# Kernel optimization log

Hardware: AMD Instinct MI355X
Metric: run time of the kernel (lower is better)

## Reference

```python
import jax, jax.numpy as jnp
import numpy as np

B, V, D, K = 32, 4096, 64, 512


def setup_inputs() -> dict:
    key = jax.random.key(0)
    k1, k2 = jax.random.split(key)
    z_e = jax.random.normal(k1, (B, V, D), dtype=jnp.float32)
    # nn.Embedding weight initialized uniform(-1/K, 1/K)
    emb = jax.random.uniform(k2, (K, D), dtype=jnp.float32, minval=-1.0 / K, maxval=1.0 / K)
    return {"z_e": z_e, "emb": emb}


def reference(z_e, emb):
    b, v, d = z_e.shape
    flat = z_e.reshape(-1, d)  # [N, D], N = B*V
    # Squared Euclidean distances via dot-product expansion.
    # torch.cdist returns sqrt of this, but argmin is identical (monotone sqrt).
    d2 = (
        jnp.sum(flat * flat, axis=-1, keepdims=True)  # [N, 1]
        - 2.0 * flat @ emb.T                          # [N, K]
        + jnp.sum(emb * emb, axis=-1)                 # [K]
    )
    indices = jnp.argmin(d2, axis=1)                  # [N]
    z_q = emb[indices].reshape(z_e.shape)             # [B, V, D]
    z_q_st = z_e + jax.lax.stop_gradient(z_q - z_e)   # straight-through
    return z_q_st, z_q, indices.reshape(b, v)
```

## Files before the change

### kernel.cpp

```cpp
#include <hip/hip_runtime.h>


#define VQ_N (32 * 4096)
#define VQ_D 64
#define VQ_K 512

__device__ __forceinline__ float freeze(float x) {
  asm volatile("" : "+v"(x));
  return x;
}

__global__ __launch_bounds__(256) void vq_norms_kernel(
    const float* __restrict__ emb, float* __restrict__ nrm) {
  int k = blockIdx.x * blockDim.x + threadIdx.x;
  if (k < VQ_K) {
    const float* e = emb + k * VQ_D;
    float r0 = freeze(e[0] * e[0]), r1 = freeze(e[1] * e[1]);
    float r2 = freeze(e[2] * e[2]), r3 = freeze(e[3] * e[3]);
    float r4 = freeze(e[4] * e[4]), r5 = freeze(e[5] * e[5]);
    float r6 = freeze(e[6] * e[6]), r7 = freeze(e[7] * e[7]);
#pragma unroll
    for (int i = 8; i < VQ_D; i += 8) {
      r0 += freeze(e[i + 0] * e[i + 0]); r1 += freeze(e[i + 1] * e[i + 1]);
      r2 += freeze(e[i + 2] * e[i + 2]); r3 += freeze(e[i + 3] * e[i + 3]);
      r4 += freeze(e[i + 4] * e[i + 4]); r5 += freeze(e[i + 5] * e[i + 5]);
      r6 += freeze(e[i + 6] * e[i + 6]); r7 += freeze(e[i + 7] * e[i + 7]);
    }
    nrm[k] = ((r0 + r1) + (r2 + r3)) + ((r4 + r5) + (r6 + r7));
  }
}

__global__ __launch_bounds__(256) void vq_main_kernel(
    const float* __restrict__ z_e, const float* __restrict__ emb,
    const float* __restrict__ nrm, float* __restrict__ out_st,
    float* __restrict__ out_q, float* __restrict__ out_idx) {
  __shared__ float4 z_lds[16][64];
  __shared__ float s_val[256];
  __shared__ int s_idx[256];
  __shared__ int s_best[64];

  const int tid = threadIdx.x;
  const int lane = tid & 63;
  const int chunk = __builtin_amdgcn_readfirstlane(tid >> 6);
  const int row0 = blockIdx.x * 64;
  const int row = row0 + lane;

  const float4* zg = (const float4*)(z_e + (size_t)row0 * VQ_D);
#pragma unroll
  for (int t = 0; t < 4; ++t) {
    int i = t * 256 + tid;
    z_lds[i & 15][i >> 4] = zg[i];
  }
  __syncthreads();

  float r0, r1, r2, r3, r4, r5, r6, r7;
  {
    float4 p0 = z_lds[0][lane], p1 = z_lds[1][lane];
    r0 = freeze(p0.x * p0.x); r1 = freeze(p0.y * p0.y);
    r2 = freeze(p0.z * p0.z); r3 = freeze(p0.w * p0.w);
    r4 = freeze(p1.x * p1.x); r5 = freeze(p1.y * p1.y);
    r6 = freeze(p1.z * p1.z); r7 = freeze(p1.w * p1.w);
#pragma unroll
    for (int c = 2; c < 16; c += 2) {
      float4 q0 = z_lds[c][lane], q1 = z_lds[c + 1][lane];
      r0 += freeze(q0.x * q0.x); r1 += freeze(q0.y * q0.y);
      r2 += freeze(q0.z * q0.z); r3 += freeze(q0.w * q0.w);
      r4 += freeze(q1.x * q1.x); r5 += freeze(q1.y * q1.y);
      r6 += freeze(q1.z * q1.z); r7 += freeze(q1.w * q1.w);
    }
  }
  const float A = ((r0 + r1) + (r2 + r3)) + ((r4 + r5) + (r6 + r7));

  const int k0 = chunk * (VQ_K / 4);
  float bestv = 3.4e38f;
  int best = k0;
  for (int kk = k0; kk < k0 + VQ_K / 4; kk += 8) {
    const float* e0 = emb + (size_t)(kk + 0) * VQ_D;
    const float* e1 = emb + (size_t)(kk + 1) * VQ_D;
    const float* e2 = emb + (size_t)(kk + 2) * VQ_D;
    const float* e3 = emb + (size_t)(kk + 3) * VQ_D;
    const float* e4 = emb + (size_t)(kk + 4) * VQ_D;
    const float* e5 = emb + (size_t)(kk + 5) * VQ_D;
    const float* e6 = emb + (size_t)(kk + 6) * VQ_D;
    const float* e7 = emb + (size_t)(kk + 7) * VQ_D;
    float a0 = 0.f, a1 = 0.f, a2 = 0.f, a3 = 0.f;
    float a4 = 0.f, a5 = 0.f, a6 = 0.f, a7 = 0.f;
#pragma unroll
    for (int c = 0; c < 16; ++c) {
      float4 zc = z_lds[c][lane];
      a0 = fmaf(zc.x, e0[4 * c + 0], a0); a0 = fmaf(zc.y, e0[4 * c + 1], a0);
      a0 = fmaf(zc.z, e0[4 * c + 2], a0); a0 = fmaf(zc.w, e0[4 * c + 3], a0);
      a1 = fmaf(zc.x, e1[4 * c + 0], a1); a1 = fmaf(zc.y, e1[4 * c + 1], a1);
      a1 = fmaf(zc.z, e1[4 * c + 2], a1); a1 = fmaf(zc.w, e1[4 * c + 3], a1);
      a2 = fmaf(zc.x, e2[4 * c + 0], a2); a2 = fmaf(zc.y, e2[4 * c + 1], a2);
      a2 = fmaf(zc.z, e2[4 * c + 2], a2); a2 = fmaf(zc.w, e2[4 * c + 3], a2);
      a3 = fmaf(zc.x, e3[4 * c + 0], a3); a3 = fmaf(zc.y, e3[4 * c + 1], a3);
      a3 = fmaf(zc.z, e3[4 * c + 2], a3); a3 = fmaf(zc.w, e3[4 * c + 3], a3);
      a4 = fmaf(zc.x, e4[4 * c + 0], a4); a4 = fmaf(zc.y, e4[4 * c + 1], a4);
      a4 = fmaf(zc.z, e4[4 * c + 2], a4); a4 = fmaf(zc.w, e4[4 * c + 3], a4);
      a5 = fmaf(zc.x, e5[4 * c + 0], a5); a5 = fmaf(zc.y, e5[4 * c + 1], a5);
      a5 = fmaf(zc.z, e5[4 * c + 2], a5); a5 = fmaf(zc.w, e5[4 * c + 3], a5);
      a6 = fmaf(zc.x, e6[4 * c + 0], a6); a6 = fmaf(zc.y, e6[4 * c + 1], a6);
      a6 = fmaf(zc.z, e6[4 * c + 2], a6); a6 = fmaf(zc.w, e6[4 * c + 3], a6);
      a7 = fmaf(zc.x, e7[4 * c + 0], a7); a7 = fmaf(zc.y, e7[4 * c + 1], a7);
      a7 = fmaf(zc.z, e7[4 * c + 2], a7); a7 = fmaf(zc.w, e7[4 * c + 3], a7);
    }
    float t0 = fmaf(-2.0f, a0, A) + nrm[kk + 0];
    float t1 = fmaf(-2.0f, a1, A) + nrm[kk + 1];
    float t2 = fmaf(-2.0f, a2, A) + nrm[kk + 2];
    float t3 = fmaf(-2.0f, a3, A) + nrm[kk + 3];
    float t4 = fmaf(-2.0f, a4, A) + nrm[kk + 4];
    float t5 = fmaf(-2.0f, a5, A) + nrm[kk + 5];
    float t6 = fmaf(-2.0f, a6, A) + nrm[kk + 6];
    float t7 = fmaf(-2.0f, a7, A) + nrm[kk + 7];
    if (t0 < bestv) { bestv = t0; best = kk + 0; }
    if (t1 < bestv) { bestv = t1; best = kk + 1; }
    if (t2 < bestv) { bestv = t2; best = kk + 2; }
    if (t3 < bestv) { bestv = t3; best = kk + 3; }
    if (t4 < bestv) { bestv = t4; best = kk + 4; }
    if (t5 < bestv) { bestv = t5; best = kk + 5; }
    if (t6 < bestv) { bestv = t6; best = kk + 6; }
    if (t7 < bestv) { bestv = t7; best = kk + 7; }
  }

  s_val[chunk * 64 + lane] = bestv;
  s_idx[chunk * 64 + lane] = best;
  __syncthreads();

  if (tid < 64) {
    float v = s_val[tid];
    int b = s_idx[tid];
#pragma unroll
    for (int c = 1; c < 4; ++c) {
      float vc = s_val[c * 64 + tid];
      if (vc < v) { v = vc; b = s_idx[c * 64 + tid]; }
    }
    s_best[tid] = b;
    out_idx[row] = (float)b;
  }
  __syncthreads();

  const float4* eg4 = (const float4*)emb;
  const size_t base4 = (size_t)blockIdx.x * 64 * 16;
  float4* o0 = (float4*)out_st;
  float4* o1 = (float4*)out_q;
#pragma unroll
  for (int t = 0; t < 4; ++t) {
    int i = t * 256 + tid;
    int r = i >> 4, j = i & 15;
    float4 v = eg4[s_best[r] * 16 + j];
    o0[base4 + i] = v;
    o1[base4 + i] = v;
  }
}

extern "C" void kernel_launch(void* const* d_in, const int* in_sizes, int n_in,
                              void* d_out, int out_size, void* d_ws,
                              size_t ws_size, hipStream_t stream) {
  const float* z_e = (const float*)d_in[0];
  const float* emb = (const float*)d_in[1];
  float* nrm = (float*)d_ws;

  float* out_st = (float*)d_out;
  float* out_q = out_st + (size_t)VQ_N * VQ_D;
  float* out_idx = out_q + (size_t)VQ_N * VQ_D;

  vq_norms_kernel<<<(VQ_K + 255) / 256, 256, 0, stream>>>(emb, nrm);
  vq_main_kernel<<<VQ_N / 64, 256, 0, stream>>>(z_e, emb, nrm, out_st, out_q,
                                                out_idx);
}
```

Baseline: 237.4 us.

## Stage codebook tiles in LDS and interleave codes across waves

Codebook rows were previously read by each wave straight from global memory as scalar loads. Now the block copies the codebook into LDS in tiles of 64 codes and each wave computes 16 codes per tile, so every wave covers a strided subset of the whole codebook. This costs extra block-wide barriers and LDS traffic, in exchange for coalesced loads and reuse across waves. The final reduction across waves gains a tie-break on the lower index, which keeps argmin semantics now that the code ranges interleave.

```diff
diff --git a/kernel.cpp b/kernel.cpp
--- a/kernel.cpp
+++ b/kernel.cpp
@@ -35,13 +35,14 @@
     const float* __restrict__ nrm, float* __restrict__ out_st,
     float* __restrict__ out_q, float* __restrict__ out_idx) {
   __shared__ float4 z_lds[16][64];
+  __shared__ float4 e_lds[64 * 16];
   __shared__ float s_val[256];
   __shared__ int s_idx[256];
   __shared__ int s_best[64];
 
   const int tid = threadIdx.x;
   const int lane = tid & 63;
-  const int chunk = __builtin_amdgcn_readfirstlane(tid >> 6);
+  const int wave = __builtin_amdgcn_readfirstlane(tid >> 6);
   const int row0 = blockIdx.x * 64;
   const int row = row0 + lane;
 
@@ -71,60 +72,57 @@
   }
   const float A = ((r0 + r1) + (r2 + r3)) + ((r4 + r5) + (r6 + r7));
 
-  const int k0 = chunk * (VQ_K / 4);
   float bestv = 3.4e38f;
-  int best = k0;
-  for (int kk = k0; kk < k0 + VQ_K / 4; kk += 8) {
-    const float* e0 = emb + (size_t)(kk + 0) * VQ_D;
-    const float* e1 = emb + (size_t)(kk + 1) * VQ_D;
-    const float* e2 = emb + (size_t)(kk + 2) * VQ_D;
-    const float* e3 = emb + (size_t)(kk + 3) * VQ_D;
-    const float* e4 = emb + (size_t)(kk + 4) * VQ_D;
-    const float* e5 = emb + (size_t)(kk + 5) * VQ_D;
-    const float* e6 = emb + (size_t)(kk + 6) * VQ_D;
-    const float* e7 = emb + (size_t)(kk + 7) * VQ_D;
-    float a0 = 0.f, a1 = 0.f, a2 = 0.f, a3 = 0.f;
-    float a4 = 0.f, a5 = 0.f, a6 = 0.f, a7 = 0.f;
+  int best = 0;
+
+  for (int t = 0; t < 8; ++t) {
+    const float4* eg = (const float4*)emb + (size_t)t * 1024;
 #pragma unroll
-    for (int c = 0; c < 16; ++c) {
-      float4 zc = z_lds[c][lane];
-      a0 = fmaf(zc.x, e0[4 * c + 0], a0); a0 = fmaf(zc.y, e0[4 * c + 1], a0);
-      a0 = fmaf(zc.z, e0[4 * c + 2], a0); a0 = fmaf(zc.w, e0[4 * c + 3], a0);
-      a1 = fmaf(zc.x, e1[4 * c + 0], a1); a1 = fmaf(zc.y, e1[4 * c + 1], a1);
-      a1 = fmaf(zc.z, e1[4 * c + 2], a1); a1 = fmaf(zc.w, e1[4 * c + 3], a1);
-      a2 = fmaf(zc.x, e2[4 * c + 0], a2); a2 = fmaf(zc.y, e2[4 * c + 1], a2);
-      a2 = fmaf(zc.z, e2[4 * c + 2], a2); a2 = fmaf(zc.w, e2[4 * c + 3], a2);
-      a3 = fmaf(zc.x, e3[4 * c + 0], a3); a3 = fmaf(zc.y, e3[4 * c + 1], a3);
-      a3 = fmaf(zc.z, e3[4 * c + 2], a3); a3 = fmaf(zc.w, e3[4 * c + 3], a3);
-      a4 = fmaf(zc.x, e4[4 * c + 0], a4); a4 = fmaf(zc.y, e4[4 * c + 1], a4);
-      a4 = fmaf(zc.z, e4[4 * c + 2], a4); a4 = fmaf(zc.w, e4[4 * c + 3], a4);
-      a5 = fmaf(zc.x, e5[4 * c + 0], a5); a5 = fmaf(zc.y, e5[4 * c + 1], a5);
-      a5 = fmaf(zc.z, e5[4 * c + 2], a5); a5 = fmaf(zc.w, e5[4 * c + 3], a5);
-      a6 = fmaf(zc.x, e6[4 * c + 0], a6); a6 = fmaf(zc.y, e6[4 * c + 1], a6);
-      a6 = fmaf(zc.z, e6[4 * c + 2], a6); a6 = fmaf(zc.w, e6[4 * c + 3], a6);
-      a7 = fmaf(zc.x, e7[4 * c + 0], a7); a7 = fmaf(zc.y, e7[4 * c + 1], a7);
-      a7 = fmaf(zc.z, e7[4 * c + 2], a7); a7 = fmaf(zc.w, e7[4 * c + 3], a7);
+    for (int i = 0; i < 4; ++i) e_lds[i * 256 + tid] = eg[i * 256 + tid];
+    __syncthreads();
+
+#pragma unroll
+    for (int g = 0; g < 2; ++g) {
+      const int kl = wave * 16 + g * 8;
+      const int kk = t * 64 + kl;
+      const float4* ep = &e_lds[kl * 16];
+      float a0 = 0.f, a1 = 0.f, a2 = 0.f, a3 = 0.f;
+      float a4 = 0.f, a5 = 0.f, a6 = 0.f, a7 = 0.f;
+#define VQ_DOT4(ACC, J)                                                  \
+  do {                                                                   \
+    float4 f = ep[(J)*16 + c];                                           \
+    ACC = fmaf(zc.x, f.x, ACC); ACC = fmaf(zc.y, f.y, ACC);              \
+    ACC = fmaf(zc.z, f.z, ACC); ACC = fmaf(zc.w, f.w, ACC);              \
+  } while (0)
+#pragma unroll
+      for (int c = 0; c < 16; ++c) {
+        float4 zc = z_lds[c][lane];
+        VQ_DOT4(a0, 0); VQ_DOT4(a1, 1); VQ_DOT4(a2, 2); VQ_DOT4(a3, 3);
+        VQ_DOT4(a4, 4); VQ_DOT4(a5, 5); VQ_DOT4(a6, 6); VQ_DOT4(a7, 7);
+      }
+#undef VQ_DOT4
+      float t0 = fmaf(-2.0f, a0, A) + nrm[kk + 0];
+      float t1 = fmaf(-2.0f, a1, A) + nrm[kk + 1];
+      float t2 = fmaf(-2.0f, a2, A) + nrm[kk + 2];
+      float t3 = fmaf(-2.0f, a3, A) + nrm[kk + 3];
+      float t4 = fmaf(-2.0f, a4, A) + nrm[kk + 4];
+      float t5 = fmaf(-2.0f, a5, A) + nrm[kk + 5];
+      float t6 = fmaf(-2.0f, a6, A) + nrm[kk + 6];
+      float t7 = fmaf(-2.0f, a7, A) + nrm[kk + 7];
+      if (t0 < bestv) { bestv = t0; best = kk + 0; }
+      if (t1 < bestv) { bestv = t1; best = kk + 1; }
+      if (t2 < bestv) { bestv = t2; best = kk + 2; }
+      if (t3 < bestv) { bestv = t3; best = kk + 3; }
+      if (t4 < bestv) { bestv = t4; best = kk + 4; }
+      if (t5 < bestv) { bestv = t5; best = kk + 5; }
+      if (t6 < bestv) { bestv = t6; best = kk + 6; }
+      if (t7 < bestv) { bestv = t7; best = kk + 7; }
     }
-    float t0 = fmaf(-2.0f, a0, A) + nrm[kk + 0];
-    float t1 = fmaf(-2.0f, a1, A) + nrm[kk + 1];
-    float t2 = fmaf(-2.0f, a2, A) + nrm[kk + 2];
-    float t3 = fmaf(-2.0f, a3, A) + nrm[kk + 3];
-    float t4 = fmaf(-2.0f, a4, A) + nrm[kk + 4];
-    float t5 = fmaf(-2.0f, a5, A) + nrm[kk + 5];
-    float t6 = fmaf(-2.0f, a6, A) + nrm[kk + 6];
-    float t7 = fmaf(-2.0f, a7, A) + nrm[kk + 7];
-    if (t0 < bestv) { bestv = t0; best = kk + 0; }
-    if (t1 < bestv) { bestv = t1; best = kk + 1; }
-    if (t2 < bestv) { bestv = t2; best = kk + 2; }
-    if (t3 < bestv) { bestv = t3; best = kk + 3; }
-    if (t4 < bestv) { bestv = t4; best = kk + 4; }
-    if (t5 < bestv) { bestv = t5; best = kk + 5; }
-    if (t6 < bestv) { bestv = t6; best = kk + 6; }
-    if (t7 < bestv) { bestv = t7; best = kk + 7; }
+    __syncthreads();
   }
 
-  s_val[chunk * 64 + lane] = bestv;
-  s_idx[chunk * 64 + lane] = best;
+  s_val[wave * 64 + lane] = bestv;
+  s_idx[wave * 64 + lane] = best;
   __syncthreads();
 
   if (tid < 64) {
@@ -133,7 +131,8 @@
 #pragma unroll
     for (int c = 1; c < 4; ++c) {
       float vc = s_val[c * 64 + tid];
-      if (vc < v) { v = vc; b = s_idx[c * 64 + tid]; }
+      int bc = s_idx[c * 64 + tid];
+      if (vc < v || (vc == v && bc < b)) { v = vc; b = bc; }
     }
     s_best[tid] = b;
     out_idx[row] = (float)b;
```

Result: slower. 262.2 us (+10.5%).
